# Performance work log

Measured on AMD Instinct MI355X. Metric: run time of the kernel, lower is better.

The kernel has to match this reference:

```python
import jax, jax.numpy as jnp
import numpy as np

B, S, D, H = 2, 2048, 1024, 16
HD = D // H  # head_dim = 64

def setup_inputs() -> dict:
    key = jax.random.key(0)
    ks = jax.random.split(key, 5)
    scale = 1.0 / np.sqrt(D)
    x = jax.random.normal(ks[0], (B, S, D), dtype=jnp.float32)
    Wq = jax.random.normal(ks[1], (D, D), dtype=jnp.float32) * scale
    Wk = jax.random.normal(ks[2], (D, D), dtype=jnp.float32) * scale
    Wv = jax.random.normal(ks[3], (D, D), dtype=jnp.float32) * scale
    Wf = jax.random.normal(ks[4], (D, D), dtype=jnp.float32) * scale
    z = jnp.zeros((D,), dtype=jnp.float32)
    return {"x": x, "Wq": Wq, "bq": z, "Wk": Wk, "bk": z, "Wv": Wv, "bv": z, "Wf": Wf, "bf": z}

def reference(x, Wq, bq, Wk, bk, Wv, bv, Wf, bf):
    # Linear layers follow torch convention: y = x @ W.T + b
    def split_heads(t):  # [B,S,D] -> [B,H,S,HD]
        return t.reshape(B, S, H, HD).transpose(0, 2, 1, 3)
    q = split_heads(x @ Wq.T + bq)
    k = split_heads(x @ Wk.T + bk)
    v = split_heads(x @ Wv.T + bv)
    scores = jnp.einsum('bhqd,bhkd->bhqk', q, k) / jnp.sqrt(jnp.float32(HD))
    causal = jnp.tril(jnp.ones((S, S), dtype=bool))  # [S,S]
    scores = jnp.where(causal[None, None], scores, -jnp.inf)
    attn = jax.nn.softmax(scores, axis=-1)
    out = jnp.einsum('bhqk,bhkd->bhqd', attn, v)
    out = out.transpose(0, 2, 1, 3).reshape(B, S, D)
    return out @ Wf.T + bf
```

## Files before the change

kernel.cpp:

```cpp
#include <hip/hip_runtime.h>
#include <stdint.h>

#define B_  2
#define S_  2048
#define D_  1024
#define H_  16
#define HD_ 64
#define M_  (B_*S_)

typedef __bf16 bf16x8 __attribute__((ext_vector_type(8)));
typedef float  f32x4  __attribute__((ext_vector_type(4)));

typedef const __attribute__((address_space(1))) void* gas_ptr;
typedef __attribute__((address_space(3))) void* las_ptr;

__device__ __forceinline__ uint16_t f32_to_bf16(float f) {
  uint32_t u = __float_as_uint(f);
  u += 0x7FFFu + ((u >> 16) & 1u);
  return (uint16_t)(u >> 16);
}

__device__ __forceinline__ uint16_t f32_to_bf16_rtz(float f) {
  return (uint16_t)(__float_as_uint(f) >> 16);
}

__device__ __forceinline__ void g2l16(const uint16_t* g, uint16_t* l) {
  __builtin_amdgcn_global_load_lds((gas_ptr)g, (las_ptr)l, 16, 0, 0);
}

__device__ __forceinline__ int swz_src(int s) {
  return (s >> 2) * D_ + (((s & 3) ^ ((s >> 3) & 3)) * 8);
}

__global__ void cast_all(const float* __restrict__ x,
                         const float* __restrict__ wq, const float* __restrict__ wk,
                         const float* __restrict__ wv, const float* __restrict__ wf,
                         uint16_t* __restrict__ xb,
                         uint16_t* __restrict__ wqb, uint16_t* __restrict__ wkb,
                         uint16_t* __restrict__ wvb, uint16_t* __restrict__ wfb) {
  const int X4 = M_ * D_ / 4;
  const int W4 = D_ * D_ / 4;
  int i = blockIdx.x * 256 + threadIdx.x;
  const float* src; uint16_t* dst; int off;
  if (i < X4) { src = x; dst = xb; off = i; }
  else {
    int j = i - X4;
    int w = j >> 18;
    off = j & (W4 - 1);
    src = (w == 0) ? wq : (w == 1) ? wk : (w == 2) ? wv : wf;
    dst = (w == 0) ? wqb : (w == 1) ? wkb : (w == 2) ? wvb : wfb;
  }
  float4 v = ((const float4*)src)[off];
  ushort4 o;
  o.x = f32_to_bf16(v.x); o.y = f32_to_bf16(v.y);
  o.z = f32_to_bf16(v.z); o.w = f32_to_bf16(v.w);
  ((ushort4*)dst)[off] = o;
}

__global__ __launch_bounds__(512, 2)
void qkv_gemm(const uint16_t* __restrict__ xb,
              const uint16_t* __restrict__ wqb, const uint16_t* __restrict__ wkb,
              const uint16_t* __restrict__ wvb,
              const float* __restrict__ bqv, const float* __restrict__ bkv,
              const float* __restrict__ bvv,
              uint16_t* __restrict__ qout, uint16_t* __restrict__ kout,
              uint16_t* __restrict__ vtout)
{
  __shared__ __align__(16) uint16_t As[2][2][8192];
  __shared__ __align__(16) uint16_t Bs[2][2][8192];

  const int wsel = blockIdx.x >> 2;
  const int nsel = blockIdx.x & 3;
  const int mtile = blockIdx.y;
  const int tid  = threadIdx.x;
  const int lane = tid & 63, wave = tid >> 6;
  const int quad = lane >> 4, l16 = lane & 15;
  const int wm = (wave >> 2) * 128;
  const int wn = (wave & 3) * 64;
  const int sw = quad ^ ((l16 >> 1) & 3);

  const uint16_t *Ap, *Bp;
  int m0e, n0e;
  if (wsel < 2) {
    Ap = xb; Bp = (wsel == 0) ? wqb : wkb;
    m0e = mtile * 256; n0e = nsel * 256;
  } else {
    Ap = wvb; Bp = xb;
    m0e = nsel * 256; n0e = mtile * 256;
  }

  const int so0 = swz_src(tid);
  const int so1 = swz_src(tid + 512);
  const uint16_t* gA = Ap + (size_t)m0e * D_;
  const uint16_t* gB = Bp + (size_t)n0e * D_;
  const int d0 = (wave * 64) * 8;
  const int d1 = (512 + wave * 64) * 8;

  f32x4 acc[8][4];
  #pragma unroll
  for (int i = 0; i < 8; ++i)
    #pragma unroll
    for (int j = 0; j < 4; ++j)
      #pragma unroll
      for (int e = 0; e < 4; ++e)
        acc[i][j][e] = 0.f;

  g2l16(gA + so0,      &As[0][0][d0]);
  g2l16(gA + so1,      &As[0][0][d1]);
  g2l16(gB + so0,      &Bs[0][0][d0]);
  g2l16(gB + so1,      &Bs[0][0][d1]);
  g2l16(gA + 32 + so0, &As[0][1][d0]);
  g2l16(gA + 32 + so1, &As[0][1][d1]);
  g2l16(gB + 32 + so0, &Bs[0][1][d0]);
  g2l16(gB + 32 + so1, &Bs[0][1][d1]);
  asm volatile("s_waitcnt vmcnt(4)" ::: "memory");
  __builtin_amdgcn_s_barrier();

  bf16x8 bfr[4], afr[4];
  for (int t = 0; t < 16; ++t) {
    const int c = t & 1, cn = c ^ 1;
    const bool pf = (t < 15);
    const int kn = (t + 1) * 64;
    #pragma unroll
    for (int h = 0; h < 2; ++h) {
      #pragma unroll
      for (int nt = 0; nt < 4; ++nt) {
        const int ro = ((wn + nt * 16 + l16) * 4 + sw) * 8;
        bfr[nt] = *(const bf16x8*)(&Bs[c][h][ro]);
      }
      #pragma unroll
      for (int i = 0; i < 4; ++i) {
        const int ro = ((wm + i * 16 + l16) * 4 + sw) * 8;
        afr[i] = *(const bf16x8*)(&As[c][h][ro]);
      }
      if (pf) {
        g2l16(gA + kn + h * 32 + so0, &As[cn][h][d0]);
        g2l16(gA + kn + h * 32 + so1, &As[cn][h][d1]);
        g2l16(gB + kn + h * 32 + so0, &Bs[cn][h][d0]);
        g2l16(gB + kn + h * 32 + so1, &Bs[cn][h][d1]);
      }
      __builtin_amdgcn_s_barrier();
      asm volatile("s_waitcnt lgkmcnt(0)" ::: "memory");
      __builtin_amdgcn_sched_barrier(0);
      __builtin_amdgcn_s_setprio(1);
      #pragma unroll
      for (int i = 0; i < 4; ++i)
        #pragma unroll
        for (int nt = 0; nt < 4; ++nt)
          acc[i][nt] = __builtin_amdgcn_mfma_f32_16x16x32_bf16(
              afr[i], bfr[nt], acc[i][nt], 0, 0, 0);
      __builtin_amdgcn_s_setprio(0);
      __builtin_amdgcn_s_barrier();

      #pragma unroll
      for (int i = 0; i < 4; ++i) {
        const int ro = ((wm + (4 + i) * 16 + l16) * 4 + sw) * 8;
        afr[i] = *(const bf16x8*)(&As[c][h][ro]);
      }
      __builtin_amdgcn_s_barrier();
      asm volatile("s_waitcnt lgkmcnt(0)" ::: "memory");
      __builtin_amdgcn_sched_barrier(0);
      __builtin_amdgcn_s_setprio(1);
      #pragma unroll
      for (int i = 0; i < 4; ++i)
        #pragma unroll
        for (int nt = 0; nt < 4; ++nt)
          acc[4 + i][nt] = __builtin_amdgcn_mfma_f32_16x16x32_bf16(
              afr[i], bfr[nt], acc[4 + i][nt], 0, 0, 0);
      __builtin_amdgcn_s_setprio(0);
      if (h == 0) {
        if (pf) asm volatile("s_waitcnt vmcnt(8)" ::: "memory");
        else    asm volatile("s_waitcnt vmcnt(0)" ::: "memory");
      } else {
        asm volatile("s_waitcnt vmcnt(4)" ::: "memory");
      }
      __builtin_amdgcn_s_barrier();
    }
  }

  if (wsel < 2) {
    const float* bias = (wsel == 0) ? bqv : bkv;
    uint16_t* outp = (wsel == 0) ? qout : kout;
    const float scl = (wsel == 0) ? 0.18033688f : 1.0f;
    #pragma unroll
    for (int nt = 0; nt < 4; ++nt) {
      const int n = n0e + wn + nt * 16 + l16;
      const int h = n >> 6, hd = n & 63;
      const float bia = bias[n];
      #pragma unroll
      for (int mt = 0; mt < 8; ++mt) {
        #pragma unroll
        for (int r = 0; r < 4; ++r) {
          const int m = m0e + wm + mt * 16 + quad * 4 + r;
          const int bb = m >> 11, s = m & (S_ - 1);
          outp[(((size_t)(bb * H_ + h)) * S_ + s) * HD_ + hd] =
              f32_to_bf16((acc[mt][nt][r] + bia) * scl);
        }
      }
    }
  } else {
    #pragma unroll
    for (int mt = 0; mt < 8; ++mt) {
      #pragma unroll
      for (int r = 0; r < 4; ++r) {
        const int m = m0e + wm + mt * 16 + quad * 4 + r;
        const int h = m >> 6, hd = m & 63;
        const float bia = bvv[m];
        #pragma unroll
        for (int nt = 0; nt < 4; ++nt) {
          const int n = n0e + wn + nt * 16 + l16;
          const int bb = n >> 11, s = n & (S_ - 1);
          vtout[(((size_t)(bb * H_ + h)) * HD_ + hd) * S_ + s] =
              f32_to_bf16(acc[mt][nt][r] + bia);
        }
      }
    }
  }
}

__global__ __launch_bounds__(256)
void flash_attn(const uint16_t* __restrict__ qb, const uint16_t* __restrict__ kb,
                const uint16_t* __restrict__ vtb, uint16_t* __restrict__ ao)
{
  __shared__ __align__(16) uint16_t ks[2][2][2048];
  __shared__ __align__(16) uint16_t vs[2][2][2048];
  __shared__ __align__(16) uint16_t p_lds[4][16][72];

  const int bh = blockIdx.x;
  const int qt = (int)(gridDim.y - 1u - blockIdx.y);
  const int wave = threadIdx.x >> 6, lane = threadIdx.x & 63;
  const int quad = lane >> 4, l16 = lane & 15;
  const int sw = quad ^ ((l16 >> 1) & 3);
  const int q0 = qt * 64;

  const uint16_t* Q  = qb  + (size_t)bh * S_ * HD_;
  const uint16_t* Kp = kb  + (size_t)bh * S_ * HD_;
  const uint16_t* Vt = vtb + (size_t)bh * HD_ * S_;

  const int qrow = q0 + wave * 16;
  bf16x8 aq0 = *(const bf16x8*)(Q + (size_t)(qrow + l16) * HD_ + quad * 8);
  bf16x8 aq1 = *(const bf16x8*)(Q + (size_t)(qrow + l16) * HD_ + 32 + quad * 8);

  const int srow = lane >> 2;
  const int schk = (lane & 3) ^ ((lane >> 3) & 3);
  const uint16_t* sb[4]; uint16_t* sd0[4]; uint16_t* sd1[4]; int sstep[4];
  #pragma unroll
  for (int j = 0; j < 4; ++j) {
    const int g = wave * 4 + j;
    if (g < 8) {
      const int c = (g >> 2) & 1, rb = g & 3;
      sd0[j] = &ks[0][c][rb * 512];
      sd1[j] = &ks[1][c][rb * 512];
      sb[j] = Kp + (size_t)(rb * 16 + srow) * HD_ + c * 32 + schk * 8;
      sstep[j] = 64 * HD_;
    } else {
      const int gg = g - 8, c = (gg >> 2) & 1, rb = gg & 3;
      sd0[j] = &vs[0][c][rb * 512];
      sd1[j] = &vs[1][c][rb * 512];
      sb[j] = Vt + (size_t)(rb * 16 + srow) * S_ + c * 32 + schk * 8;
      sstep[j] = 64;
    }
  }

  float lpart[4];
  f32x4 o[4];
  #pragma unroll
  for (int r = 0; r < 4; ++r) lpart[r] = 0.f;
  #pragma unroll
  for (int t = 0; t < 4; ++t)
    #pragma unroll
    for (int e = 0; e < 4; ++e) o[t][e] = 0.f;

  const int rowid = qrow + quad * 4;

  #pragma unroll
  for (int j = 0; j < 4; ++j) {
    g2l16(sb[j], sd0[j]);
    sb[j] += sstep[j];
  }
  __syncthreads();

  for (int kt = 0; kt <= qt; ++kt) {
    const int kbase = kt * 64;
    const bool diag = (kt == qt);
    const int cb = kt & 1;

    if (kt < qt) {
      #pragma unroll
      for (int j = 0; j < 4; ++j) {
        g2l16(sb[j], cb ? sd0[j] : sd1[j]);
        sb[j] += sstep[j];
      }
    }

    bf16x8 kf0[4], kf1[4];
    #pragma unroll
    for (int nt = 0; nt < 4; ++nt) {
      kf0[nt] = *(const bf16x8*)(&ks[cb][0][((nt * 16 + l16) * 4 + sw) * 8]);
      kf1[nt] = *(const bf16x8*)(&ks[cb][1][((nt * 16 + l16) * 4 + sw) * 8]);
    }
    f32x4 sacc[4];
    __builtin_amdgcn_s_setprio(1);
    #pragma unroll
    for (int nt = 0; nt < 4; ++nt) {
      #pragma unroll
      for (int e = 0; e < 4; ++e) sacc[nt][e] = 0.f;
      sacc[nt] = __builtin_amdgcn_mfma_f32_16x16x32_bf16(aq0, kf0[nt], sacc[nt], 0, 0, 0);
      sacc[nt] = __builtin_amdgcn_mfma_f32_16x16x32_bf16(aq1, kf1[nt], sacc[nt], 0, 0, 0);
    }
    __builtin_amdgcn_s_setprio(0);

    bf16x8 vf0[4], vf1[4];
    #pragma unroll
    for (int t = 0; t < 4; ++t) {
      vf0[t] = *(const bf16x8*)(&vs[cb][0][((t * 16 + l16) * 4 + sw) * 8]);
      vf1[t] = *(const bf16x8*)(&vs[cb][1][((t * 16 + l16) * 4 + sw) * 8]);
    }

    #pragma unroll
    for (int nt = 0; nt < 4; ++nt) {
      const int kkc = kbase + nt * 16 + l16;
      #pragma unroll
      for (int r = 0; r < 4; ++r) {
        float p = __builtin_amdgcn_exp2f(sacc[nt][r]);
        if (diag && (kkc > rowid + r)) p = 0.f;
        lpart[r] += p;
        p_lds[wave][quad * 4 + r][nt * 16 + l16] = f32_to_bf16_rtz(p);
      }
    }

    bf16x8 ap0 = *(const bf16x8*)(&p_lds[wave][l16][quad * 8]);
    bf16x8 ap1 = *(const bf16x8*)(&p_lds[wave][l16][32 + quad * 8]);
    __builtin_amdgcn_s_setprio(1);
    #pragma unroll
    for (int t = 0; t < 4; ++t) {
      o[t] = __builtin_amdgcn_mfma_f32_16x16x32_bf16(ap0, vf0[t], o[t], 0, 0, 0);
      o[t] = __builtin_amdgcn_mfma_f32_16x16x32_bf16(ap1, vf1[t], o[t], 0, 0, 0);
    }
    __builtin_amdgcn_s_setprio(0);
    __syncthreads();
  }

  #pragma unroll
  for (int r = 0; r < 4; ++r) {
    lpart[r] += __shfl_xor(lpart[r], 1, 64);
    lpart[r] += __shfl_xor(lpart[r], 2, 64);
    lpart[r] += __shfl_xor(lpart[r], 4, 64);
    lpart[r] += __shfl_xor(lpart[r], 8, 64);
  }
  const int bb = bh >> 4, h = bh & 15;
  #pragma unroll
  for (int t = 0; t < 4; ++t) {
    #pragma unroll
    for (int r = 0; r < 4; ++r) {
      const float ov = o[t][r] / lpart[r];
      ao[((size_t)(bb * S_ + rowid + r)) * D_ + h * HD_ + t * 16 + l16] =
          f32_to_bf16(ov);
    }
  }
}

__global__ __launch_bounds__(256)
void out_gemm(const uint16_t* __restrict__ ab, const uint16_t* __restrict__ wfb,
              const float* __restrict__ bfv, float* __restrict__ out)
{
  __shared__ __align__(16) uint16_t As[2 * 64 * 32];
  __shared__ __align__(16) uint16_t Bs[2 * 128 * 32];
  const int m0 = blockIdx.y * 64;
  const int n0 = blockIdx.x * 128;
  const int lane = threadIdx.x & 63, wave = threadIdx.x >> 6;
  const int quad = lane >> 4, l16 = lane & 15;
  const int wm = (wave >> 1) * 32, wn = (wave & 1) * 64;
  const int sw = quad ^ ((l16 >> 1) & 3);

  f32x4 acc[2][4];
  #pragma unroll
  for (int i = 0; i < 2; ++i)
    #pragma unroll
    for (int j = 0; j < 4; ++j)
      #pragma unroll
      for (int e = 0; e < 4; ++e)
        acc[i][j][e] = 0.f;

  const int sA  = wave * 64 + lane;
  const int sB1 = sA + 256;
  const int soA = swz_src(sA), soB1 = swz_src(sB1);
  uint16_t* lA  = As + (size_t)(wave * 64) * 8;
  uint16_t* lB0 = Bs + (size_t)(wave * 64) * 8;
  uint16_t* lB1 = Bs + (size_t)(256 + wave * 64) * 8;
  const uint16_t* gA  = ab  + (size_t)m0 * D_ + soA;
  const uint16_t* gB0 = wfb + (size_t)n0 * D_ + soA;
  const uint16_t* gB1 = wfb + (size_t)n0 * D_ + soB1;

  for (int k0 = 0; k0 < D_; k0 += 64) {
    g2l16(gA  + k0,      lA);
    g2l16(gB0 + k0,      lB0);
    g2l16(gB1 + k0,      lB1);
    g2l16(gA  + k0 + 32, lA  + 2048);
    g2l16(gB0 + k0 + 32, lB0 + 4096);
    g2l16(gB1 + k0 + 32, lB1 + 4096);
    __syncthreads();
    bf16x8 af0[2], af1[2], bf0[4], bf1[4];
    #pragma unroll
    for (int mt = 0; mt < 2; ++mt) {
      const int ro = ((wm + mt * 16 + l16) * 4 + sw) * 8;
      af0[mt] = *(const bf16x8*)(As + ro);
      af1[mt] = *(const bf16x8*)(As + 2048 + ro);
    }
    #pragma unroll
    for (int nt = 0; nt < 4; ++nt) {
      const int ro = ((wn + nt * 16 + l16) * 4 + sw) * 8;
      bf0[nt] = *(const bf16x8*)(Bs + ro);
      bf1[nt] = *(const bf16x8*)(Bs + 4096 + ro);
    }
    #pragma unroll
    for (int mt = 0; mt < 2; ++mt)
      #pragma unroll
      for (int nt = 0; nt < 4; ++nt) {
        acc[mt][nt] = __builtin_amdgcn_mfma_f32_16x16x32_bf16(
            af0[mt], bf0[nt], acc[mt][nt], 0, 0, 0);
        acc[mt][nt] = __builtin_amdgcn_mfma_f32_16x16x32_bf16(
            af1[mt], bf1[nt], acc[mt][nt], 0, 0, 0);
      }
    __syncthreads();
  }

  #pragma unroll
  for (int nt = 0; nt < 4; ++nt) {
    const int n = n0 + wn + nt * 16 + l16;
    const float bia = bfv[n];
    #pragma unroll
    for (int mt = 0; mt < 2; ++mt) {
      #pragma unroll
      for (int r = 0; r < 4; ++r) {
        const int m = m0 + wm + mt * 16 + quad * 4 + r;
        out[(size_t)m * D_ + n] = acc[mt][nt][r] + bia;
      }
    }
  }
}

extern "C" void kernel_launch(void* const* d_in, const int* in_sizes, int n_in,
                              void* d_out, int out_size, void* d_ws, size_t ws_size,
                              hipStream_t stream) {
  (void)in_sizes; (void)n_in; (void)out_size; (void)ws_size;
  const float* x  = (const float*)d_in[0];
  const float* Wq = (const float*)d_in[1];
  const float* bq = (const float*)d_in[2];
  const float* Wk = (const float*)d_in[3];
  const float* bk = (const float*)d_in[4];
  const float* Wv = (const float*)d_in[5];
  const float* bv = (const float*)d_in[6];
  const float* Wf = (const float*)d_in[7];
  const float* bf = (const float*)d_in[8];
  float* out = (float*)d_out;

  uint16_t* ws = (uint16_t*)d_ws;
  uint16_t* xb   = ws;
  uint16_t* wqb  = xb  + (size_t)M_ * D_;
  uint16_t* wkb  = wqb + (size_t)D_ * D_;
  uint16_t* wvb  = wkb + (size_t)D_ * D_;
  uint16_t* wfb  = wvb + (size_t)D_ * D_;
  uint16_t* qbuf = wfb + (size_t)D_ * D_;
  uint16_t* kbuf = qbuf + (size_t)M_ * D_;
  uint16_t* vtb  = kbuf + (size_t)M_ * D_;
  uint16_t* aob  = vtb  + (size_t)M_ * D_;

  const int CAST_BLOCKS = (M_ * D_ / 4 + 4 * (D_ * D_ / 4)) / 256;
  cast_all<<<CAST_BLOCKS, 256, 0, stream>>>(x, Wq, Wk, Wv, Wf,
                                            xb, wqb, wkb, wvb, wfb);

  qkv_gemm<<<dim3(12, 16), 512, 0, stream>>>(xb, wqb, wkb, wvb, bq, bk, bv,
                                             qbuf, kbuf, vtb);
  flash_attn<<<dim3(32, 32), 256, 0, stream>>>(qbuf, kbuf, vtb, aob);
  out_gemm<<<dim3(8, 64), 256, 0, stream>>>(aob, wfb, bf, out);
}
```

Before: 181.5 us.

## Software-pipeline LDS fragment loads in QKV GEMM and double-buffer output GEMM

In the QKV projection GEMM, the per-half barriers are replaced by a register-level pipeline. Fragments for the next MFMA group are read from LDS while the current group computes, using partial lgkmcnt waits, and the whole next K-tile is prefetched at once with a single barrier per iteration. The output GEMM gets double-buffered LDS, so global-to-LDS copies for the next K step overlap the MFMAs on the current one, plus raised wave priority around the MFMAs. This cuts barrier and load-latency stalls at the cost of more registers and more LDS.

```diff
diff --git a/kernel.cpp b/kernel.cpp
--- a/kernel.cpp
+++ b/kernel.cpp
@@ -105,76 +105,102 @@
       for (int e = 0; e < 4; ++e)
         acc[i][j][e] = 0.f;
 
-  g2l16(gA + so0,      &As[0][0][d0]);
-  g2l16(gA + so1,      &As[0][0][d1]);
-  g2l16(gB + so0,      &Bs[0][0][d0]);
-  g2l16(gB + so1,      &Bs[0][0][d1]);
-  g2l16(gA + 32 + so0, &As[0][1][d0]);
-  g2l16(gA + 32 + so1, &As[0][1][d1]);
-  g2l16(gB + 32 + so0, &Bs[0][1][d0]);
-  g2l16(gB + 32 + so1, &Bs[0][1][d1]);
-  asm volatile("s_waitcnt vmcnt(4)" ::: "memory");
+  #pragma unroll
+  for (int h2 = 0; h2 < 2; ++h2) {
+    g2l16(gA + h2 * 32 + so0, &As[0][h2][d0]);
+    g2l16(gA + h2 * 32 + so1, &As[0][h2][d1]);
+    g2l16(gB + h2 * 32 + so0, &Bs[0][h2][d0]);
+    g2l16(gB + h2 * 32 + so1, &Bs[0][h2][d1]);
+  }
+  asm volatile("s_waitcnt vmcnt(0)" ::: "memory");
   __builtin_amdgcn_s_barrier();
 
-  bf16x8 bfr[4], afr[4];
+  bf16x8 bfr[2][4], af03[2][4], af47[2][4];
+  #pragma unroll
+  for (int nt = 0; nt < 4; ++nt)
+    bfr[0][nt] = *(const bf16x8*)(&Bs[0][0][((wn + nt * 16 + l16) * 4 + sw) * 8]);
+  #pragma unroll
+  for (int i = 0; i < 4; ++i)
+    af03[0][i] = *(const bf16x8*)(&As[0][0][((wm + i * 16 + l16) * 4 + sw) * 8]);
+
   for (int t = 0; t < 16; ++t) {
     const int c = t & 1, cn = c ^ 1;
     const bool pf = (t < 15);
     const int kn = (t + 1) * 64;
-    #pragma unroll
-    for (int h = 0; h < 2; ++h) {
-      #pragma unroll
-      for (int nt = 0; nt < 4; ++nt) {
-        const int ro = ((wn + nt * 16 + l16) * 4 + sw) * 8;
-        bfr[nt] = *(const bf16x8*)(&Bs[c][h][ro]);
-      }
-      #pragma unroll
-      for (int i = 0; i < 4; ++i) {
-        const int ro = ((wm + i * 16 + l16) * 4 + sw) * 8;
-        afr[i] = *(const bf16x8*)(&As[c][h][ro]);
-      }
-      if (pf) {
-        g2l16(gA + kn + h * 32 + so0, &As[cn][h][d0]);
-        g2l16(gA + kn + h * 32 + so1, &As[cn][h][d1]);
-        g2l16(gB + kn + h * 32 + so0, &Bs[cn][h][d0]);
-        g2l16(gB + kn + h * 32 + so1, &Bs[cn][h][d1]);
-      }
+
+    #pragma unroll
+    for (int i = 0; i < 4; ++i)
+      af47[0][i] = *(const bf16x8*)(&As[c][0][((wm + (4 + i) * 16 + l16) * 4 + sw) * 8]);
+    if (pf) {
+      #pragma unroll
+      for (int h2 = 0; h2 < 2; ++h2) {
+        g2l16(gA + kn + h2 * 32 + so0, &As[cn][h2][d0]);
+        g2l16(gA + kn + h2 * 32 + so1, &As[cn][h2][d1]);
+        g2l16(gB + kn + h2 * 32 + so0, &Bs[cn][h2][d0]);
+        g2l16(gB + kn + h2 * 32 + so1, &Bs[cn][h2][d1]);
+      }
+    }
+    asm volatile("s_waitcnt lgkmcnt(4)" ::: "memory");
+    __builtin_amdgcn_sched_barrier(0);
+    __builtin_amdgcn_s_setprio(1);
+    #pragma unroll
+    for (int i = 0; i < 4; ++i)
+      #pragma unroll
+      for (int nt = 0; nt < 4; ++nt)
+        acc[i][nt] = __builtin_amdgcn_mfma_f32_16x16x32_bf16(
+            af03[0][i], bfr[0][nt], acc[i][nt], 0, 0, 0);
+    __builtin_amdgcn_s_setprio(0);
+
+    #pragma unroll
+    for (int nt = 0; nt < 4; ++nt)
+      bfr[1][nt] = *(const bf16x8*)(&Bs[c][1][((wn + nt * 16 + l16) * 4 + sw) * 8]);
+    #pragma unroll
+    for (int i = 0; i < 4; ++i)
+      af03[1][i] = *(const bf16x8*)(&As[c][1][((wm + i * 16 + l16) * 4 + sw) * 8]);
+    asm volatile("s_waitcnt lgkmcnt(8)" ::: "memory");
+    __builtin_amdgcn_sched_barrier(0);
+    __builtin_amdgcn_s_setprio(1);
+    #pragma unroll
+    for (int i = 0; i < 4; ++i)
+      #pragma unroll
+      for (int nt = 0; nt < 4; ++nt)
+        acc[4 + i][nt] = __builtin_amdgcn_mfma_f32_16x16x32_bf16(
+            af47[0][i], bfr[0][nt], acc[4 + i][nt], 0, 0, 0);
+    __builtin_amdgcn_s_setprio(0);
+
+    #pragma unroll
+    for (int i = 0; i < 4; ++i)
+      af47[1][i] = *(const bf16x8*)(&As[c][1][((wm + (4 + i) * 16 + l16) * 4 + sw) * 8]);
+    asm volatile("s_waitcnt lgkmcnt(4)" ::: "memory");
+    __builtin_amdgcn_sched_barrier(0);
+    __builtin_amdgcn_s_setprio(1);
+    #pragma unroll
+    for (int i = 0; i < 4; ++i)
+      #pragma unroll
+      for (int nt = 0; nt < 4; ++nt)
+        acc[i][nt] = __builtin_amdgcn_mfma_f32_16x16x32_bf16(
+            af03[1][i], bfr[1][nt], acc[i][nt], 0, 0, 0);
+    __builtin_amdgcn_s_setprio(0);
+
+    asm volatile("s_waitcnt lgkmcnt(0)" ::: "memory");
+    __builtin_amdgcn_sched_barrier(0);
+    __builtin_amdgcn_s_setprio(1);
+    #pragma unroll
+    for (int i = 0; i < 4; ++i)
+      #pragma unroll
+      for (int nt = 0; nt < 4; ++nt)
+        acc[4 + i][nt] = __builtin_amdgcn_mfma_f32_16x16x32_bf16(
+            af47[1][i], bfr[1][nt], acc[4 + i][nt], 0, 0, 0);
+    __builtin_amdgcn_s_setprio(0);
+    if (pf) {
+      asm volatile("s_waitcnt vmcnt(0)" ::: "memory");
       __builtin_amdgcn_s_barrier();
-      asm volatile("s_waitcnt lgkmcnt(0)" ::: "memory");
-      __builtin_amdgcn_sched_barrier(0);
-      __builtin_amdgcn_s_setprio(1);
+      #pragma unroll
+      for (int nt = 0; nt < 4; ++nt)
+        bfr[0][nt] = *(const bf16x8*)(&Bs[cn][0][((wn + nt * 16 + l16) * 4 + sw) * 8]);
       #pragma unroll
       for (int i = 0; i < 4; ++i)
-        #pragma unroll
-        for (int nt = 0; nt < 4; ++nt)
-          acc[i][nt] = __builtin_amdgcn_mfma_f32_16x16x32_bf16(
-              afr[i], bfr[nt], acc[i][nt], 0, 0, 0);
-      __builtin_amdgcn_s_setprio(0);
-      __builtin_amdgcn_s_barrier();
-
-      #pragma unroll
-      for (int i = 0; i < 4; ++i) {
-        const int ro = ((wm + (4 + i) * 16 + l16) * 4 + sw) * 8;
-        afr[i] = *(const bf16x8*)(&As[c][h][ro]);
-      }
-      __builtin_amdgcn_s_barrier();
-      asm volatile("s_waitcnt lgkmcnt(0)" ::: "memory");
-      __builtin_amdgcn_sched_barrier(0);
-      __builtin_amdgcn_s_setprio(1);
-      #pragma unroll
-      for (int i = 0; i < 4; ++i)
-        #pragma unroll
-        for (int nt = 0; nt < 4; ++nt)
-          acc[4 + i][nt] = __builtin_amdgcn_mfma_f32_16x16x32_bf16(
-              afr[i], bfr[nt], acc[4 + i][nt], 0, 0, 0);
-      __builtin_amdgcn_s_setprio(0);
-      if (h == 0) {
-        if (pf) asm volatile("s_waitcnt vmcnt(8)" ::: "memory");
-        else    asm volatile("s_waitcnt vmcnt(0)" ::: "memory");
-      } else {
-        asm volatile("s_waitcnt vmcnt(4)" ::: "memory");
-      }
-      __builtin_amdgcn_s_barrier();
+        af03[0][i] = *(const bf16x8*)(&As[cn][0][((wm + i * 16 + l16) * 4 + sw) * 8]);
     }
   }
 
@@ -364,8 +390,8 @@
 void out_gemm(const uint16_t* __restrict__ ab, const uint16_t* __restrict__ wfb,
               const float* __restrict__ bfv, float* __restrict__ out)
 {
-  __shared__ __align__(16) uint16_t As[2 * 64 * 32];
-  __shared__ __align__(16) uint16_t Bs[2 * 128 * 32];
+  __shared__ __align__(16) uint16_t As[2][2][2048];
+  __shared__ __align__(16) uint16_t Bs[2][2][4096];
   const int m0 = blockIdx.y * 64;
   const int n0 = blockIdx.x * 128;
   const int lane = threadIdx.x & 63, wave = threadIdx.x >> 6;
@@ -385,34 +411,45 @@
   const int sA  = wave * 64 + lane;
   const int sB1 = sA + 256;
   const int soA = swz_src(sA), soB1 = swz_src(sB1);
-  uint16_t* lA  = As + (size_t)(wave * 64) * 8;
-  uint16_t* lB0 = Bs + (size_t)(wave * 64) * 8;
-  uint16_t* lB1 = Bs + (size_t)(256 + wave * 64) * 8;
+  const int dA  = (wave * 64) * 8;
+  const int dB1 = (256 + wave * 64) * 8;
   const uint16_t* gA  = ab  + (size_t)m0 * D_ + soA;
   const uint16_t* gB0 = wfb + (size_t)n0 * D_ + soA;
   const uint16_t* gB1 = wfb + (size_t)n0 * D_ + soB1;
 
-  for (int k0 = 0; k0 < D_; k0 += 64) {
-    g2l16(gA  + k0,      lA);
-    g2l16(gB0 + k0,      lB0);
-    g2l16(gB1 + k0,      lB1);
-    g2l16(gA  + k0 + 32, lA  + 2048);
-    g2l16(gB0 + k0 + 32, lB0 + 4096);
-    g2l16(gB1 + k0 + 32, lB1 + 4096);
-    __syncthreads();
+  g2l16(gA,       &As[0][0][dA]);
+  g2l16(gA  + 32, &As[0][1][dA]);
+  g2l16(gB0,      &Bs[0][0][dA]);
+  g2l16(gB0 + 32, &Bs[0][1][dA]);
+  g2l16(gB1,      &Bs[0][0][dB1]);
+  g2l16(gB1 + 32, &Bs[0][1][dB1]);
+  __syncthreads();
+
+  for (int t = 0; t < 16; ++t) {
+    const int cb = t & 1, cn = cb ^ 1;
+    if (t < 15) {
+      const int kn = (t + 1) * 64;
+      g2l16(gA  + kn,      &As[cn][0][dA]);
+      g2l16(gA  + kn + 32, &As[cn][1][dA]);
+      g2l16(gB0 + kn,      &Bs[cn][0][dA]);
+      g2l16(gB0 + kn + 32, &Bs[cn][1][dA]);
+      g2l16(gB1 + kn,      &Bs[cn][0][dB1]);
+      g2l16(gB1 + kn + 32, &Bs[cn][1][dB1]);
+    }
     bf16x8 af0[2], af1[2], bf0[4], bf1[4];
     #pragma unroll
     for (int mt = 0; mt < 2; ++mt) {
       const int ro = ((wm + mt * 16 + l16) * 4 + sw) * 8;
-      af0[mt] = *(const bf16x8*)(As + ro);
-      af1[mt] = *(const bf16x8*)(As + 2048 + ro);
+      af0[mt] = *(const bf16x8*)(&As[cb][0][ro]);
+      af1[mt] = *(const bf16x8*)(&As[cb][1][ro]);
     }
     #pragma unroll
     for (int nt = 0; nt < 4; ++nt) {
       const int ro = ((wn + nt * 16 + l16) * 4 + sw) * 8;
-      bf0[nt] = *(const bf16x8*)(Bs + ro);
-      bf1[nt] = *(const bf16x8*)(Bs + 4096 + ro);
-    }
+      bf0[nt] = *(const bf16x8*)(&Bs[cb][0][ro]);
+      bf1[nt] = *(const bf16x8*)(&Bs[cb][1][ro]);
+    }
+    __builtin_amdgcn_s_setprio(1);
     #pragma unroll
     for (int mt = 0; mt < 2; ++mt)
       #pragma unroll
@@ -422,6 +459,7 @@
         acc[mt][nt] = __builtin_amdgcn_mfma_f32_16x16x32_bf16(
             af1[mt], bf1[nt], acc[mt][nt], 0, 0, 0);
       }
+    __builtin_amdgcn_s_setprio(0);
     __syncthreads();
   }
 
```

Measured after the change: 179.0 us. About the same (-1.4%).

## Pre-pack bf16 operands into swizzled tile layout and retile GEMMs to 128x128

Applied to the files above, without the earlier changes.

The cast kernel now writes x and the weights into a tile-packed, pre-swizzled layout, and flash attention writes its output in the same layout. Each 128-row by 32-column LDS tile then becomes one contiguous global block that loads with simple linear offsets. The QKV GEMM moves from 256x256 tiles with 512 threads to 128x128 tiles with 256 threads (768 blocks), dropping the manual two-phase waitcnt pipeline for a simpler double buffer with __syncthreads. The output GEMM moves from 64x128 to 128x128 tiles. This gives more blocks and more coalesced loads, at the cost of less reuse per block and a simpler pipeline.

```diff
diff --git a/kernel.cpp b/kernel.cpp
--- a/kernel.cpp
+++ b/kernel.cpp
@@ -10,6 +10,7 @@
 
 typedef __bf16 bf16x8 __attribute__((ext_vector_type(8)));
 typedef float  f32x4  __attribute__((ext_vector_type(4)));
+typedef unsigned short u16x8 __attribute__((ext_vector_type(8)));
 
 typedef const __attribute__((address_space(1))) void* gas_ptr;
 typedef __attribute__((address_space(3))) void* las_ptr;
@@ -28,36 +29,42 @@
   __builtin_amdgcn_global_load_lds((gas_ptr)g, (las_ptr)l, 16, 0, 0);
 }
 
-__device__ __forceinline__ int swz_src(int s) {
-  return (s >> 2) * D_ + (((s & 3) ^ ((s >> 3) & 3)) * 8);
-}
-
-__global__ void cast_all(const float* __restrict__ x,
-                         const float* __restrict__ wq, const float* __restrict__ wk,
-                         const float* __restrict__ wv, const float* __restrict__ wf,
-                         uint16_t* __restrict__ xb,
-                         uint16_t* __restrict__ wqb, uint16_t* __restrict__ wkb,
-                         uint16_t* __restrict__ wvb, uint16_t* __restrict__ wfb) {
-  const int X4 = M_ * D_ / 4;
-  const int W4 = D_ * D_ / 4;
+#define POFF(rt, kt, h) ((size_t)((((rt) * 16 + (kt)) * 2 + (h)) * 4096))
+
+__global__ void cast_pack(const float* __restrict__ x,
+                          const float* __restrict__ wq, const float* __restrict__ wk,
+                          const float* __restrict__ wv, const float* __restrict__ wf,
+                          uint16_t* __restrict__ xb,
+                          uint16_t* __restrict__ wqb, uint16_t* __restrict__ wkb,
+                          uint16_t* __restrict__ wvb, uint16_t* __restrict__ wfb) {
+  const int XC = M_ * D_ / 8;
+  const int WC = D_ * D_ / 8;
   int i = blockIdx.x * 256 + threadIdx.x;
   const float* src; uint16_t* dst; int off;
-  if (i < X4) { src = x; dst = xb; off = i; }
+  if (i < XC) { src = x; dst = xb; off = i; }
   else {
-    int j = i - X4;
-    int w = j >> 18;
-    off = j & (W4 - 1);
+    int j = i - XC;
+    int w = j >> 17;
+    off = j & (WC - 1);
     src = (w == 0) ? wq : (w == 1) ? wk : (w == 2) ? wv : wf;
     dst = (w == 0) ? wqb : (w == 1) ? wkb : (w == 2) ? wvb : wfb;
   }
-  float4 v = ((const float4*)src)[off];
-  ushort4 o;
-  o.x = f32_to_bf16(v.x); o.y = f32_to_bf16(v.y);
-  o.z = f32_to_bf16(v.z); o.w = f32_to_bf16(v.w);
-  ((ushort4*)dst)[off] = o;
-}
-
-__global__ __launch_bounds__(512, 2)
+  const int row = off >> 7;
+  const int c   = off & 127;
+  const float4 v0 = ((const float4*)src)[row * 256 + c * 2];
+  const float4 v1 = ((const float4*)src)[row * 256 + c * 2 + 1];
+  u16x8 o;
+  o[0] = f32_to_bf16(v0.x); o[1] = f32_to_bf16(v0.y);
+  o[2] = f32_to_bf16(v0.z); o[3] = f32_to_bf16(v0.w);
+  o[4] = f32_to_bf16(v1.x); o[5] = f32_to_bf16(v1.y);
+  o[6] = f32_to_bf16(v1.z); o[7] = f32_to_bf16(v1.w);
+  const int kt = c >> 3, c8 = c & 7, h = c8 >> 2, c4 = c8 & 3;
+  const int rt = row >> 7, r = row & 127;
+  const int s = 4 * r + (c4 ^ ((r >> 1) & 3));
+  *(u16x8*)(dst + POFF(rt, kt, h) + s * 8) = o;
+}
+
+__global__ __launch_bounds__(256, 2)
 void qkv_gemm(const uint16_t* __restrict__ xb,
               const uint16_t* __restrict__ wqb, const uint16_t* __restrict__ wkb,
               const uint16_t* __restrict__ wvb,
@@ -66,116 +73,87 @@
               uint16_t* __restrict__ qout, uint16_t* __restrict__ kout,
               uint16_t* __restrict__ vtout)
 {
-  __shared__ __align__(16) uint16_t As[2][2][8192];
-  __shared__ __align__(16) uint16_t Bs[2][2][8192];
-
-  const int wsel = blockIdx.x >> 2;
-  const int nsel = blockIdx.x & 3;
+  __shared__ __align__(16) uint16_t As[2][2][4096];
+  __shared__ __align__(16) uint16_t Bs[2][2][4096];
+
+  const int wsel = blockIdx.x >> 3;
+  const int nsel = blockIdx.x & 7;
   const int mtile = blockIdx.y;
   const int tid  = threadIdx.x;
   const int lane = tid & 63, wave = tid >> 6;
   const int quad = lane >> 4, l16 = lane & 15;
-  const int wm = (wave >> 2) * 128;
-  const int wn = (wave & 3) * 64;
+  const int wm = (wave >> 1) * 64, wn = (wave & 1) * 64;
   const int sw = quad ^ ((l16 >> 1) & 3);
 
   const uint16_t *Ap, *Bp;
-  int m0e, n0e;
+  int art, brt, m0e, n0e;
   if (wsel < 2) {
-    Ap = xb; Bp = (wsel == 0) ? wqb : wkb;
-    m0e = mtile * 256; n0e = nsel * 256;
+    Ap = xb; art = mtile; Bp = (wsel == 0) ? wqb : wkb; brt = nsel;
+    m0e = mtile * 128; n0e = nsel * 128;
   } else {
-    Ap = wvb; Bp = xb;
-    m0e = nsel * 256; n0e = mtile * 256;
-  }
-
-  const int so0 = swz_src(tid);
-  const int so1 = swz_src(tid + 512);
-  const uint16_t* gA = Ap + (size_t)m0e * D_;
-  const uint16_t* gB = Bp + (size_t)n0e * D_;
-  const int d0 = (wave * 64) * 8;
-  const int d1 = (512 + wave * 64) * 8;
-
-  f32x4 acc[8][4];
-  #pragma unroll
-  for (int i = 0; i < 8; ++i)
+    Ap = wvb; art = nsel; Bp = xb; brt = mtile;
+    m0e = nsel * 128; n0e = mtile * 128;
+  }
+
+  const int se0 = tid * 8;
+  const int se1 = (256 + tid) * 8;
+  const int ld0 = (wave * 64) * 8;
+  const int ld1 = (256 + wave * 64) * 8;
+
+  f32x4 acc[4][4];
+  #pragma unroll
+  for (int i = 0; i < 4; ++i)
     #pragma unroll
     for (int j = 0; j < 4; ++j)
       #pragma unroll
       for (int e = 0; e < 4; ++e)
         acc[i][j][e] = 0.f;
 
-  g2l16(gA + so0,      &As[0][0][d0]);
-  g2l16(gA + so1,      &As[0][0][d1]);
-  g2l16(gB + so0,      &Bs[0][0][d0]);
-  g2l16(gB + so1,      &Bs[0][0][d1]);
-  g2l16(gA + 32 + so0, &As[0][1][d0]);
-  g2l16(gA + 32 + so1, &As[0][1][d1]);
-  g2l16(gB + 32 + so0, &Bs[0][1][d0]);
-  g2l16(gB + 32 + so1, &Bs[0][1][d1]);
-  asm volatile("s_waitcnt vmcnt(4)" ::: "memory");
-  __builtin_amdgcn_s_barrier();
-
-  bf16x8 bfr[4], afr[4];
+  #pragma unroll
+  for (int h = 0; h < 2; ++h) {
+    g2l16(Ap + POFF(art, 0, h) + se0, &As[0][h][ld0]);
+    g2l16(Ap + POFF(art, 0, h) + se1, &As[0][h][ld1]);
+    g2l16(Bp + POFF(brt, 0, h) + se0, &Bs[0][h][ld0]);
+    g2l16(Bp + POFF(brt, 0, h) + se1, &Bs[0][h][ld1]);
+  }
+  __syncthreads();
+
   for (int t = 0; t < 16; ++t) {
-    const int c = t & 1, cn = c ^ 1;
-    const bool pf = (t < 15);
-    const int kn = (t + 1) * 64;
-    #pragma unroll
-    for (int h = 0; h < 2; ++h) {
+    const int cb = t & 1, cn = cb ^ 1;
+    if (t < 15) {
+      #pragma unroll
+      for (int h = 0; h < 2; ++h) {
+        g2l16(Ap + POFF(art, t + 1, h) + se0, &As[cn][h][ld0]);
+        g2l16(Ap + POFF(art, t + 1, h) + se1, &As[cn][h][ld1]);
+        g2l16(Bp + POFF(brt, t + 1, h) + se0, &Bs[cn][h][ld0]);
+        g2l16(Bp + POFF(brt, t + 1, h) + se1, &Bs[cn][h][ld1]);
+      }
+    }
+    bf16x8 af[4][2], bf[4][2];
+    #pragma unroll
+    for (int mt = 0; mt < 4; ++mt) {
+      const int ro = ((wm + mt * 16 + l16) * 4 + sw) * 8;
+      af[mt][0] = *(const bf16x8*)(&As[cb][0][ro]);
+      af[mt][1] = *(const bf16x8*)(&As[cb][1][ro]);
+    }
+    #pragma unroll
+    for (int nt = 0; nt < 4; ++nt) {
+      const int ro = ((wn + nt * 16 + l16) * 4 + sw) * 8;
+      bf[nt][0] = *(const bf16x8*)(&Bs[cb][0][ro]);
+      bf[nt][1] = *(const bf16x8*)(&Bs[cb][1][ro]);
+    }
+    __builtin_amdgcn_s_setprio(1);
+    #pragma unroll
+    for (int mt = 0; mt < 4; ++mt)
       #pragma unroll
       for (int nt = 0; nt < 4; ++nt) {
-        const int ro = ((wn + nt * 16 + l16) * 4 + sw) * 8;
-        bfr[nt] = *(const bf16x8*)(&Bs[c][h][ro]);
-      }
-      #pragma unroll
-      for (int i = 0; i < 4; ++i) {
-        const int ro = ((wm + i * 16 + l16) * 4 + sw) * 8;
-        afr[i] = *(const bf16x8*)(&As[c][h][ro]);
-      }
-      if (pf) {
-        g2l16(gA + kn + h * 32 + so0, &As[cn][h][d0]);
-        g2l16(gA + kn + h * 32 + so1, &As[cn][h][d1]);
-        g2l16(gB + kn + h * 32 + so0, &Bs[cn][h][d0]);
-        g2l16(gB + kn + h * 32 + so1, &Bs[cn][h][d1]);
-      }
-      __builtin_amdgcn_s_barrier();
-      asm volatile("s_waitcnt lgkmcnt(0)" ::: "memory");
-      __builtin_amdgcn_sched_barrier(0);
-      __builtin_amdgcn_s_setprio(1);
-      #pragma unroll
-      for (int i = 0; i < 4; ++i)
-        #pragma unroll
-        for (int nt = 0; nt < 4; ++nt)
-          acc[i][nt] = __builtin_amdgcn_mfma_f32_16x16x32_bf16(
-              afr[i], bfr[nt], acc[i][nt], 0, 0, 0);
-      __builtin_amdgcn_s_setprio(0);
-      __builtin_amdgcn_s_barrier();
-
-      #pragma unroll
-      for (int i = 0; i < 4; ++i) {
-        const int ro = ((wm + (4 + i) * 16 + l16) * 4 + sw) * 8;
-        afr[i] = *(const bf16x8*)(&As[c][h][ro]);
-      }
-      __builtin_amdgcn_s_barrier();
-      asm volatile("s_waitcnt lgkmcnt(0)" ::: "memory");
-      __builtin_amdgcn_sched_barrier(0);
-      __builtin_amdgcn_s_setprio(1);
-      #pragma unroll
-      for (int i = 0; i < 4; ++i)
-        #pragma unroll
-        for (int nt = 0; nt < 4; ++nt)
-          acc[4 + i][nt] = __builtin_amdgcn_mfma_f32_16x16x32_bf16(
-              afr[i], bfr[nt], acc[4 + i][nt], 0, 0, 0);
-      __builtin_amdgcn_s_setprio(0);
-      if (h == 0) {
-        if (pf) asm volatile("s_waitcnt vmcnt(8)" ::: "memory");
-        else    asm volatile("s_waitcnt vmcnt(0)" ::: "memory");
-      } else {
-        asm volatile("s_waitcnt vmcnt(4)" ::: "memory");
-      }
-      __builtin_amdgcn_s_barrier();
-    }
+        acc[mt][nt] = __builtin_amdgcn_mfma_f32_16x16x32_bf16(
+            af[mt][0], bf[nt][0], acc[mt][nt], 0, 0, 0);
+        acc[mt][nt] = __builtin_amdgcn_mfma_f32_16x16x32_bf16(
+            af[mt][1], bf[nt][1], acc[mt][nt], 0, 0, 0);
+      }
+    __builtin_amdgcn_s_setprio(0);
+    __syncthreads();
   }
 
   if (wsel < 2) {
@@ -188,7 +166,7 @@
       const int h = n >> 6, hd = n & 63;
       const float bia = bias[n];
       #pragma unroll
-      for (int mt = 0; mt < 8; ++mt) {
+      for (int mt = 0; mt < 4; ++mt) {
         #pragma unroll
         for (int r = 0; r < 4; ++r) {
           const int m = m0e + wm + mt * 16 + quad * 4 + r;
@@ -200,7 +178,7 @@
     }
   } else {
     #pragma unroll
-    for (int mt = 0; mt < 8; ++mt) {
+    for (int mt = 0; mt < 4; ++mt) {
       #pragma unroll
       for (int r = 0; r < 4; ++r) {
         const int m = m0e + wm + mt * 16 + quad * 4 + r;
@@ -351,86 +329,99 @@
   const int bb = bh >> 4, h = bh & 15;
   #pragma unroll
   for (int t = 0; t < 4; ++t) {
+    const int c8 = t * 2 + (l16 >> 3);
+    const int hh = c8 >> 2, c4 = c8 & 3, e = l16 & 7;
     #pragma unroll
     for (int r = 0; r < 4; ++r) {
       const float ov = o[t][r] / lpart[r];
-      ao[((size_t)(bb * S_ + rowid + r)) * D_ + h * HD_ + t * 16 + l16] =
-          f32_to_bf16(ov);
-    }
-  }
-}
-
-__global__ __launch_bounds__(256)
+      const int grow = bb * S_ + rowid + r;
+      const int rt = grow >> 7, rr = grow & 127;
+      const int s = 4 * rr + (c4 ^ ((rr >> 1) & 3));
+      ao[POFF(rt, h, hh) + s * 8 + e] = f32_to_bf16(ov);
+    }
+  }
+}
+
+__global__ __launch_bounds__(256, 2)
 void out_gemm(const uint16_t* __restrict__ ab, const uint16_t* __restrict__ wfb,
               const float* __restrict__ bfv, float* __restrict__ out)
 {
-  __shared__ __align__(16) uint16_t As[2 * 64 * 32];
-  __shared__ __align__(16) uint16_t Bs[2 * 128 * 32];
-  const int m0 = blockIdx.y * 64;
-  const int n0 = blockIdx.x * 128;
-  const int lane = threadIdx.x & 63, wave = threadIdx.x >> 6;
+  __shared__ __align__(16) uint16_t As[2][2][4096];
+  __shared__ __align__(16) uint16_t Bs[2][2][4096];
+  const int nsel = blockIdx.x;
+  const int mtile = blockIdx.y;
+  const int tid  = threadIdx.x;
+  const int lane = tid & 63, wave = tid >> 6;
   const int quad = lane >> 4, l16 = lane & 15;
-  const int wm = (wave >> 1) * 32, wn = (wave & 1) * 64;
+  const int wm = (wave >> 1) * 64, wn = (wave & 1) * 64;
   const int sw = quad ^ ((l16 >> 1) & 3);
 
-  f32x4 acc[2][4];
-  #pragma unroll
-  for (int i = 0; i < 2; ++i)
+  const int se0 = tid * 8, se1 = (256 + tid) * 8;
+  const int ld0 = (wave * 64) * 8, ld1 = (256 + wave * 64) * 8;
+
+  f32x4 acc[4][4];
+  #pragma unroll
+  for (int i = 0; i < 4; ++i)
     #pragma unroll
     for (int j = 0; j < 4; ++j)
       #pragma unroll
       for (int e = 0; e < 4; ++e)
         acc[i][j][e] = 0.f;
 
-  const int sA  = wave * 64 + lane;
-  const int sB1 = sA + 256;
-  const int soA = swz_src(sA), soB1 = swz_src(sB1);
-  uint16_t* lA  = As + (size_t)(wave * 64) * 8;
-  uint16_t* lB0 = Bs + (size_t)(wave * 64) * 8;
-  uint16_t* lB1 = Bs + (size_t)(256 + wave * 64) * 8;
-  const uint16_t* gA  = ab  + (size_t)m0 * D_ + soA;
-  const uint16_t* gB0 = wfb + (size_t)n0 * D_ + soA;
-  const uint16_t* gB1 = wfb + (size_t)n0 * D_ + soB1;
-
-  for (int k0 = 0; k0 < D_; k0 += 64) {
-    g2l16(gA  + k0,      lA);
-    g2l16(gB0 + k0,      lB0);
-    g2l16(gB1 + k0,      lB1);
-    g2l16(gA  + k0 + 32, lA  + 2048);
-    g2l16(gB0 + k0 + 32, lB0 + 4096);
-    g2l16(gB1 + k0 + 32, lB1 + 4096);
-    __syncthreads();
-    bf16x8 af0[2], af1[2], bf0[4], bf1[4];
-    #pragma unroll
-    for (int mt = 0; mt < 2; ++mt) {
+  #pragma unroll
+  for (int h = 0; h < 2; ++h) {
+    g2l16(ab  + POFF(mtile, 0, h) + se0, &As[0][h][ld0]);
+    g2l16(ab  + POFF(mtile, 0, h) + se1, &As[0][h][ld1]);
+    g2l16(wfb + POFF(nsel, 0, h) + se0, &Bs[0][h][ld0]);
+    g2l16(wfb + POFF(nsel, 0, h) + se1, &Bs[0][h][ld1]);
+  }
+  __syncthreads();
+
+  for (int t = 0; t < 16; ++t) {
+    const int cb = t & 1, cn = cb ^ 1;
+    if (t < 15) {
+      #pragma unroll
+      for (int h = 0; h < 2; ++h) {
+        g2l16(ab  + POFF(mtile, t + 1, h) + se0, &As[cn][h][ld0]);
+        g2l16(ab  + POFF(mtile, t + 1, h) + se1, &As[cn][h][ld1]);
+        g2l16(wfb + POFF(nsel, t + 1, h) + se0, &Bs[cn][h][ld0]);
+        g2l16(wfb + POFF(nsel, t + 1, h) + se1, &Bs[cn][h][ld1]);
+      }
+    }
+    bf16x8 af[4][2], bf[4][2];
+    #pragma unroll
+    for (int mt = 0; mt < 4; ++mt) {
       const int ro = ((wm + mt * 16 + l16) * 4 + sw) * 8;
-      af0[mt] = *(const bf16x8*)(As + ro);
-      af1[mt] = *(const bf16x8*)(As + 2048 + ro);
+      af[mt][0] = *(const bf16x8*)(&As[cb][0][ro]);
+      af[mt][1] = *(const bf16x8*)(&As[cb][1][ro]);
     }
     #pragma unroll
     for (int nt = 0; nt < 4; ++nt) {
       const int ro = ((wn + nt * 16 + l16) * 4 + sw) * 8;
-      bf0[nt] = *(const bf16x8*)(Bs + ro);
-      bf1[nt] = *(const bf16x8*)(Bs + 4096 + ro);
-    }
-    #pragma unroll
-    for (int mt = 0; mt < 2; ++mt)
+      bf[nt][0] = *(const bf16x8*)(&Bs[cb][0][ro]);
+      bf[nt][1] = *(const bf16x8*)(&Bs[cb][1][ro]);
+    }
+    __builtin_amdgcn_s_setprio(1);
+    #pragma unroll
+    for (int mt = 0; mt < 4; ++mt)
       #pragma unroll
       for (int nt = 0; nt < 4; ++nt) {
         acc[mt][nt] = __builtin_amdgcn_mfma_f32_16x16x32_bf16(
-            af0[mt], bf0[nt], acc[mt][nt], 0, 0, 0);
+            af[mt][0], bf[nt][0], acc[mt][nt], 0, 0, 0);
         acc[mt][nt] = __builtin_amdgcn_mfma_f32_16x16x32_bf16(
-            af1[mt], bf1[nt], acc[mt][nt], 0, 0, 0);
-      }
+            af[mt][1], bf[nt][1], acc[mt][nt], 0, 0, 0);
+      }
+    __builtin_amdgcn_s_setprio(0);
     __syncthreads();
   }
 
+  const int m0 = mtile * 128, n0 = nsel * 128;
   #pragma unroll
   for (int nt = 0; nt < 4; ++nt) {
     const int n = n0 + wn + nt * 16 + l16;
     const float bia = bfv[n];
     #pragma unroll
-    for (int mt = 0; mt < 2; ++mt) {
+    for (int mt = 0; mt < 4; ++mt) {
       #pragma unroll
       for (int r = 0; r < 4; ++r) {
         const int m = m0 + wm + mt * 16 + quad * 4 + r;
@@ -466,12 +457,12 @@
   uint16_t* vtb  = kbuf + (size_t)M_ * D_;
   uint16_t* aob  = vtb  + (size_t)M_ * D_;
 
-  const int CAST_BLOCKS = (M_ * D_ / 4 + 4 * (D_ * D_ / 4)) / 256;
-  cast_all<<<CAST_BLOCKS, 256, 0, stream>>>(x, Wq, Wk, Wv, Wf,
-                                            xb, wqb, wkb, wvb, wfb);
-
-  qkv_gemm<<<dim3(12, 16), 512, 0, stream>>>(xb, wqb, wkb, wvb, bq, bk, bv,
+  const int CAST_BLOCKS = (M_ * D_ / 8 + 4 * (D_ * D_ / 8)) / 256;
+  cast_pack<<<CAST_BLOCKS, 256, 0, stream>>>(x, Wq, Wk, Wv, Wf,
+                                             xb, wqb, wkb, wvb, wfb);
+
+  qkv_gemm<<<dim3(24, 32), 256, 0, stream>>>(xb, wqb, wkb, wvb, bq, bk, bv,
                                              qbuf, kbuf, vtb);
   flash_attn<<<dim3(32, 32), 256, 0, stream>>>(qbuf, kbuf, vtb, aob);
-  out_gemm<<<dim3(8, 64), 256, 0, stream>>>(aob, wfb, bf, out);
-}
+  out_gemm<<<dim3(8, 32), 256, 0, stream>>>(aob, wfb, bf, out);
+}
```

Result: no change. 182.3 us (+0.4%).
